# Kernel optimization log

Hardware: AMD Instinct MI355X
Metric: run time of the kernel (lower is better)

## Reference

```python
import jax, jax.numpy as jnp
import numpy as np

HIDDEN = 1024
NUM_HEADS = 16
HEAD_DIM = HIDDEN // NUM_HEADS
EPS = 1e-05


def setup_inputs() -> dict:
    key = jax.random.key(0)
    ks = jax.random.split(key, 6)
    B, S = 4, 2048
    x = jax.random.normal(ks[0], (B, S, HIDDEN), dtype=jnp.float32)
    # trunc_normal_(std=0.02) approximated by scaled normal
    w_in = jax.random.normal(ks[1], (3 * HIDDEN, HIDDEN), dtype=jnp.float32) * 0.02
    b_in = jax.random.normal(ks[2], (3 * HIDDEN,), dtype=jnp.float32) * 0.02
    w_norm = jnp.ones((HIDDEN,), dtype=jnp.float32)
    lim = 1.0 / np.sqrt(HIDDEN)
    w_out = jax.random.uniform(ks[3], (HIDDEN, HIDDEN), dtype=jnp.float32, minval=-lim, maxval=lim)
    b_out = jax.random.uniform(ks[4], (HIDDEN,), dtype=jnp.float32, minval=-lim, maxval=lim)
    return {"x": x, "w_in": w_in, "b_in": b_in, "w_norm": w_norm, "w_out": w_out, "b_out": b_out}


def _rms_norm(x, w, eps):
    var = jnp.mean(jnp.square(x), axis=-1, keepdims=True)
    return x * jax.lax.rsqrt(var + eps) * w


def reference(x, w_in, b_in, w_norm, w_out, b_out):
    B, S, _ = x.shape
    xn = _rms_norm(x, w_norm, EPS)
    qkv = jnp.einsum('bsd,ed->bse', xn, w_in) + b_in  # [B,S,3*HIDDEN]
    q, k, v = jnp.split(qkv, 3, axis=-1)
    # [B,S,H*D] -> [B,H,S,D]
    def split_heads(t):
        return t.reshape(B, S, NUM_HEADS, HEAD_DIM).transpose(0, 2, 1, 3)
    q, k, v = split_heads(q), split_heads(k), split_heads(v)
    scale = 1.0 / np.sqrt(HEAD_DIM)
    scores = jnp.einsum('bhqd,bhkd->bhqk', q, k) * scale
    attn = jax.nn.softmax(scores, axis=-1)
    o = jnp.einsum('bhqk,bhkd->bhqd', attn, v)
    o = o.transpose(0, 2, 1, 3).reshape(B, S, HIDDEN)
    return jnp.einsum('bsd,ed->bse', o, w_out) + b_out
```

## Files before the change

### kernel.cpp

```cpp
#include <hip/hip_runtime.h>
#include <stdint.h>

typedef short bf16x4 __attribute__((ext_vector_type(4)));
typedef short bf16x8 __attribute__((ext_vector_type(8)));
typedef _Float16 f16x8 __attribute__((ext_vector_type(8)));
typedef float f32x4 __attribute__((ext_vector_type(4)));
typedef float f32x16 __attribute__((ext_vector_type(16)));
typedef unsigned int u32x4 __attribute__((ext_vector_type(4)));

#if __has_builtin(__builtin_amdgcn_exp2f)
#define EXP2 __builtin_amdgcn_exp2f
#else
#define EXP2 exp2f
#endif

__device__ __forceinline__ short f2bf(float f) {
  union { float f; uint32_t u; } v; v.f = f;
  uint32_t r = (v.u + 0x7fffu + ((v.u >> 16) & 1u)) >> 16;
  return (short)(uint16_t)r;
}

__device__ __forceinline__ unsigned cvtpk_bf16(float lo, float hi) {
  unsigned r;
  asm("v_cvt_pk_bf16_f32 %0, %1, %2" : "=v"(r) : "v"(lo), "v"(hi));
  return r;
}

__device__ __forceinline__ f32x16 zero16() {
  f32x16 z;
#pragma unroll
  for (int i = 0; i < 16; ++i) z[i] = 0.f;
  return z;
}

__device__ __forceinline__ void gld_lds16(const void* g, void* l) {
  __builtin_amdgcn_global_load_lds(
      (__attribute__((address_space(1))) const void*)g,
      (__attribute__((address_space(3))) void*)l, 16, 0, 0);
}

__global__ __launch_bounds__(256) void k_rmsnorm(const float* __restrict__ x,
                                                 const float* __restrict__ wn,
                                                 short* __restrict__ xn) {
  const int row = blockIdx.x;
  const int t = threadIdx.x;
  const float4 v = reinterpret_cast<const float4*>(x + (size_t)row * 1024)[t];
  float ss = v.x * v.x + v.y * v.y + v.z * v.z + v.w * v.w;
#pragma unroll
  for (int m = 32; m >= 1; m >>= 1) ss += __shfl_xor(ss, m, 64);
  __shared__ float red[4];
  if ((t & 63) == 0) red[t >> 6] = ss;
  __syncthreads();
  const float tot = red[0] + red[1] + red[2] + red[3];
  const float rr = rsqrtf(tot * (1.0f / 1024.0f) + 1e-5f);
  const float4 g = reinterpret_cast<const float4*>(wn)[t];
  bf16x4 o;
  o[0] = f2bf(v.x * rr * g.x);
  o[1] = f2bf(v.y * rr * g.y);
  o[2] = f2bf(v.z * rr * g.z);
  o[3] = f2bf(v.w * rr * g.w);
  reinterpret_cast<bf16x4*>(xn + (size_t)row * 1024)[t] = o;
}

__global__ __launch_bounds__(256) void k_cast_bf(const float* __restrict__ in,
                                                 short* __restrict__ out, int n4) {
  int i = blockIdx.x * 256 + threadIdx.x;
  if (i >= n4) return;
  float4 v = reinterpret_cast<const float4*>(in)[i];
  bf16x4 o;
  o[0] = f2bf(v.x); o[1] = f2bf(v.y); o[2] = f2bf(v.z); o[3] = f2bf(v.w);
  reinterpret_cast<bf16x4*>(out)[i] = o;
}

__global__ __launch_bounds__(256) void k_cast_f16(const float* __restrict__ in,
                                                  _Float16* __restrict__ out, int n4) {
  int i = blockIdx.x * 256 + threadIdx.x;
  if (i >= n4) return;
  float4 v = reinterpret_cast<const float4*>(in)[i];
  _Float16 o[4] = {(_Float16)v.x, (_Float16)v.y, (_Float16)v.z, (_Float16)v.w};
  reinterpret_cast<ulong1*>(out)[i] = *reinterpret_cast<ulong1*>(o);
}

__global__ __launch_bounds__(256) void k_gemm_qkv(const short* __restrict__ A,
                                                  const short* __restrict__ B,
                                                  const float* __restrict__ bias,
                                                  short* __restrict__ qb,
                                                  short* __restrict__ kb,
                                                  short* __restrict__ vb) {
  __shared__ __align__(16) short As[128 * 32];
  __shared__ __align__(16) short Bs[128 * 32];
  const int t = threadIdx.x;
  const long bm0 = (long)blockIdx.y * 128;
  const long bn0 = (long)blockIdx.x * 128;
  const int w = t >> 6, l = t & 63;
  const int wr = (w >> 1) * 64, wc = (w & 1) * 64;
  const int lm = l & 15, h = l >> 4;
  f32x4 acc[4][4];
#pragma unroll
  for (int i = 0; i < 4; ++i)
#pragma unroll
    for (int j = 0; j < 4; ++j) acc[i][j] = (f32x4){0.f, 0.f, 0.f, 0.f};
  const int srow = t >> 2, scol = (t & 3) * 8;
  const short* Ag = A + (bm0 + srow) * 1024 + scol;
  const short* Bg = B + (bn0 + srow) * 1024 + scol;
  short* AsP = As + t * 8;
  short* BsP = Bs + t * 8;
  for (int kt = 0; kt < 32; ++kt) {
    const int k0 = kt << 5;
    gld_lds16(Ag + k0, AsP);
    gld_lds16(Ag + k0 + 64 * 1024, AsP + 2048);
    gld_lds16(Bg + k0, BsP);
    gld_lds16(Bg + k0 + 64 * 1024, BsP + 2048);
    __syncthreads();
    bf16x8 af[4], bfr[4];
#pragma unroll
    for (int mi = 0; mi < 4; ++mi)
      af[mi] = *reinterpret_cast<const bf16x8*>(As + (wr + mi * 16 + lm) * 32 + h * 8);
#pragma unroll
    for (int ni = 0; ni < 4; ++ni)
      bfr[ni] = *reinterpret_cast<const bf16x8*>(Bs + (wc + ni * 16 + lm) * 32 + h * 8);
#pragma unroll
    for (int mi = 0; mi < 4; ++mi)
#pragma unroll
      for (int ni = 0; ni < 4; ++ni)
        acc[mi][ni] = __builtin_amdgcn_mfma_f32_16x16x32_bf16(af[mi], bfr[ni], acc[mi][ni], 0, 0, 0);
    __syncthreads();
  }
#pragma unroll
  for (int ni = 0; ni < 4; ++ni) {
    const int ncol = (int)bn0 + wc + ni * 16 + lm;
    const float bv = bias[ncol];
    const int which = ncol >> 10;
    const int e = ncol & 1023;
#pragma unroll
    for (int mi = 0; mi < 4; ++mi) {
#pragma unroll
      for (int r = 0; r < 4; ++r) {
        const long mrow = bm0 + wr + mi * 16 + h * 4 + r;
        const float val = acc[mi][ni][r] + bv;
        const long off = (((mrow >> 11) * 16 + (e >> 6)) * 2048 + (mrow & 2047)) * 64 + (e & 63);
        if (which == 0) qb[off] = f2bf(val * 0.18033688011112042f);
        else if (which == 1) kb[off] = f2bf(val);
        else vb[off] = f2bf(val);
      }
    }
  }
}

__global__ __launch_bounds__(256) void k_gemm_out(const _Float16* __restrict__ A,
                                                  const _Float16* __restrict__ B,
                                                  const float* __restrict__ bias,
                                                  float* __restrict__ outp) {
  __shared__ __align__(16) _Float16 As[128 * 32];
  __shared__ __align__(16) _Float16 Bs[128 * 32];
  const int t = threadIdx.x;
  const long bm0 = (long)blockIdx.y * 128;
  const long bn0 = (long)blockIdx.x * 128;
  const int w = t >> 6, l = t & 63;
  const int wr = (w >> 1) * 64, wc = (w & 1) * 64;
  const int lm = l & 15, h = l >> 4;
  f32x4 acc[4][4];
#pragma unroll
  for (int i = 0; i < 4; ++i)
#pragma unroll
    for (int j = 0; j < 4; ++j) acc[i][j] = (f32x4){0.f, 0.f, 0.f, 0.f};
  const int srow = t >> 2, scol = (t & 3) * 8;
  const _Float16* Ag = A + (bm0 + srow) * 1024 + scol;
  const _Float16* Bg = B + (bn0 + srow) * 1024 + scol;
  _Float16* AsP = As + t * 8;
  _Float16* BsP = Bs + t * 8;
  for (int kt = 0; kt < 32; ++kt) {
    const int k0 = kt << 5;
    gld_lds16(Ag + k0, AsP);
    gld_lds16(Ag + k0 + 64 * 1024, AsP + 2048);
    gld_lds16(Bg + k0, BsP);
    gld_lds16(Bg + k0 + 64 * 1024, BsP + 2048);
    __syncthreads();
    f16x8 af[4], bfr[4];
#pragma unroll
    for (int mi = 0; mi < 4; ++mi)
      af[mi] = *reinterpret_cast<const f16x8*>(As + (wr + mi * 16 + lm) * 32 + h * 8);
#pragma unroll
    for (int ni = 0; ni < 4; ++ni)
      bfr[ni] = *reinterpret_cast<const f16x8*>(Bs + (wc + ni * 16 + lm) * 32 + h * 8);
#pragma unroll
    for (int mi = 0; mi < 4; ++mi)
#pragma unroll
      for (int ni = 0; ni < 4; ++ni)
        acc[mi][ni] = __builtin_amdgcn_mfma_f32_16x16x32_f16(af[mi], bfr[ni], acc[mi][ni], 0, 0, 0);
    __syncthreads();
  }
#pragma unroll
  for (int ni = 0; ni < 4; ++ni) {
    const int ncol = (int)bn0 + wc + ni * 16 + lm;
    const float bv = bias[ncol];
#pragma unroll
    for (int mi = 0; mi < 4; ++mi) {
#pragma unroll
      for (int r = 0; r < 4; ++r) {
        const long mrow = bm0 + wr + mi * 16 + h * 4 + r;
        outp[mrow * 1024 + ncol] = acc[mi][ni][r] + bv;
      }
    }
  }
}

__global__ __launch_bounds__(256) void k_transpose_v(const short* __restrict__ v,
                                                     short* __restrict__ vt) {
  __shared__ short tile[64][72];
  const int bh = blockIdx.y, st = blockIdx.x;
  const int t = threadIdx.x;
  const int r = t >> 2, c0 = (t & 3) * 16;
  const short* src = v + ((size_t)(bh * 2048 + st * 64 + r)) * 64 + c0;
  bf16x8 a = *reinterpret_cast<const bf16x8*>(src);
  bf16x8 b = *reinterpret_cast<const bf16x8*>(src + 8);
#pragma unroll
  for (int j = 0; j < 8; ++j) tile[r][c0 + j] = a[j];
#pragma unroll
  for (int j = 0; j < 8; ++j) tile[r][c0 + 8 + j] = b[j];
  __syncthreads();
  __align__(16) short tmp[16];
#pragma unroll
  for (int j = 0; j < 16; ++j) tmp[j] = tile[c0 + j][r];
  short* dst = vt + ((size_t)(bh * 64 + r)) * 2048 + st * 64 + c0;
  *reinterpret_cast<bf16x8*>(dst) = *reinterpret_cast<const bf16x8*>(tmp);
  *reinterpret_cast<bf16x8*>(dst + 8) = *reinterpret_cast<const bf16x8*>(tmp + 8);
}

__global__ __launch_bounds__(256) void k_attn(const short* __restrict__ q,
                                              const short* __restrict__ k,
                                              const short* __restrict__ vt,
                                              _Float16* __restrict__ o) {
  __shared__ __align__(16) short Ks[2][4096];
  __shared__ __align__(16) short Vs[2][4096];
  const int bh = blockIdx.y;
  const int qt = blockIdx.x;
  const int t = threadIdx.x;
  const int w = t >> 6, l = t & 63;
  const int lq = l & 31, hh = l >> 5;
  const int xr = lq & 7;
  const int qrow = qt * 128 + w * 32 + lq;

  const short* qp = q + ((size_t)(bh * 2048 + qrow)) * 64 + hh * 8;
  bf16x8 qf[4];
#pragma unroll
  for (int db = 0; db < 4; ++db) qf[db] = *reinterpret_cast<const bf16x8*>(qp + db * 16);

  const int gg0 = w * 128 + l, gg1 = gg0 + 64;
  const int u0 = gg0 ^ ((gg0 >> 3) & 7);
  const int u1 = gg1 ^ ((gg1 >> 3) & 7);
  const short* kh = k + (size_t)bh * 2048 * 64;
  const short* vh = vt + (size_t)bh * 64 * 2048;
  const short* ksrc0 = kh + u0 * 8;
  const short* ksrc1 = kh + u1 * 8;
  const short* vsrc0 = vh + (gg0 >> 3) * 2048 + (u0 & 7) * 8;
  const short* vsrc1 = vh + (gg1 >> 3) * 2048 + (u1 & 7) * 8;

  int koff[2][4], voff[2][4];
#pragma unroll
  for (int ks = 0; ks < 2; ++ks)
#pragma unroll
    for (int db = 0; db < 4; ++db)
      koff[ks][db] = ((ks * 32 + lq) * 8 + ((db * 2 + hh) ^ xr)) * 8;
#pragma unroll
  for (int dt = 0; dt < 2; ++dt)
#pragma unroll
    for (int kg = 0; kg < 4; ++kg)
      voff[dt][kg] = ((dt * 32 + lq) * 8 + ((kg * 2 + hh) ^ xr)) * 8;

  f32x16 oa0 = zero16(), oa1 = zero16();
  float mr = -1e30f, lr = 0.f;

  gld_lds16(ksrc0, &Ks[0][gg0 * 8]);
  gld_lds16(ksrc1, &Ks[0][gg1 * 8]);
  gld_lds16(vsrc0, &Vs[0][gg0 * 8]);
  gld_lds16(vsrc1, &Vs[0][gg1 * 8]);
  __syncthreads();

  int cur = 0;
  for (int kt = 0; kt < 32; ++kt) {
    const int kn = (kt + 1) & 31;
    const int nb = cur ^ 1;
    gld_lds16(ksrc0 + kn * 4096, &Ks[nb][gg0 * 8]);
    gld_lds16(ksrc1 + kn * 4096, &Ks[nb][gg1 * 8]);
    gld_lds16(vsrc0 + kn * 64, &Vs[nb][gg0 * 8]);
    gld_lds16(vsrc1 + kn * 64, &Vs[nb][gg1 * 8]);

    const short* kb_ = Ks[cur];
    const short* vb_ = Vs[cur];
    f32x16 s0 = zero16(), s1 = zero16();
#pragma unroll
    for (int db = 0; db < 4; ++db) {
      bf16x8 kf = *reinterpret_cast<const bf16x8*>(kb_ + koff[0][db]);
      s0 = __builtin_amdgcn_mfma_f32_32x32x16_bf16(kf, qf[db], s0, 0, 0, 0);
    }
#pragma unroll
    for (int db = 0; db < 4; ++db) {
      bf16x8 kf = *reinterpret_cast<const bf16x8*>(kb_ + koff[1][db]);
      s1 = __builtin_amdgcn_mfma_f32_32x32x16_bf16(kf, qf[db], s1, 0, 0, 0);
    }
    float m8[8];
#pragma unroll
    for (int i = 0; i < 8; ++i)
      m8[i] = fmaxf(fmaxf(s0[i], s0[i + 8]), fmaxf(s1[i], s1[i + 8]));
    float m4a = fmaxf(m8[0], m8[4]), m4b = fmaxf(m8[1], m8[5]);
    float m4c = fmaxf(m8[2], m8[6]), m4d = fmaxf(m8[3], m8[7]);
    float tm = fmaxf(fmaxf(m4a, m4b), fmaxf(m4c, m4d));
    tm = fmaxf(tm, __shfl_xor(tm, 32, 64));
    if (!__all(tm <= mr + 8.f)) {
      const float mn = fmaxf(mr, tm);
      const float corr = EXP2(mr - mn);
      lr *= corr;
#pragma unroll
      for (int r = 0; r < 16; ++r) { oa0[r] *= corr; oa1[r] *= corr; }
      mr = mn;
    }
#pragma unroll
    for (int r = 0; r < 16; ++r) {
      s0[r] = EXP2(s0[r] - mr);
      s1[r] = EXP2(s1[r] - mr);
    }
    float a8[8];
#pragma unroll
    for (int i = 0; i < 8; ++i)
      a8[i] = (s0[i] + s0[i + 8]) + (s1[i] + s1[i + 8]);
    float ts = ((a8[0] + a8[4]) + (a8[1] + a8[5])) + ((a8[2] + a8[6]) + (a8[3] + a8[7]));
    ts += __shfl_xor(ts, 32, 64);
    lr += ts;
#pragma unroll
    for (int kg = 0; kg < 4; ++kg) {
      const f32x16& sv = (kg & 2) ? s1 : s0;
      const int b0 = (kg & 1) * 8;
      unsigned w0 = cvtpk_bf16(sv[b0 + 0], sv[b0 + 1]);
      unsigned w2 = cvtpk_bf16(sv[b0 + 4], sv[b0 + 5]);
      unsigned w1 = cvtpk_bf16(sv[b0 + 2], sv[b0 + 3]);
      unsigned w3 = cvtpk_bf16(sv[b0 + 6], sv[b0 + 7]);
      asm("v_permlane32_swap_b32 %0, %1" : "+v"(w0), "+v"(w2));
      asm("v_permlane32_swap_b32 %0, %1" : "+v"(w1), "+v"(w3));
      u32x4 pw = {w0, w1, w2, w3};
      bf16x8 pf = *reinterpret_cast<bf16x8*>(&pw);
      bf16x8 vf0 = *reinterpret_cast<const bf16x8*>(vb_ + voff[0][kg]);
      oa0 = __builtin_amdgcn_mfma_f32_32x32x16_bf16(vf0, pf, oa0, 0, 0, 0);
      bf16x8 vf1 = *reinterpret_cast<const bf16x8*>(vb_ + voff[1][kg]);
      oa1 = __builtin_amdgcn_mfma_f32_32x32x16_bf16(vf1, pf, oa1, 0, 0, 0);
    }
    __syncthreads();
    cur = nb;
  }
  const float inv = 1.0f / lr;
  const int b = bh >> 4, hd = bh & 15;
  _Float16* ob = o + ((size_t)(b * 2048 + qrow)) * 1024 + hd * 64;
#pragma unroll
  for (int r2 = 0; r2 < 16; ++r2) {
    const int d0 = (r2 & 3) + 8 * (r2 >> 2) + 4 * hh;
    ob[d0] = (_Float16)(oa0[r2] * inv);
    ob[d0 + 32] = (_Float16)(oa1[r2] * inv);
  }
}

extern "C" void kernel_launch(void* const* d_in, const int* in_sizes, int n_in,
                              void* d_out, int out_size, void* d_ws, size_t ws_size,
                              hipStream_t stream) {
  const float* x = (const float*)d_in[0];
  const float* w_in = (const float*)d_in[1];
  const float* b_in = (const float*)d_in[2];
  const float* w_norm = (const float*)d_in[3];
  const float* w_out = (const float*)d_in[4];
  const float* b_out = (const float*)d_in[5];
  float* out = (float*)d_out;
  char* ws = (char*)d_ws;
  short* xn = (short*)(ws);
  short* win_b = (short*)(ws + 16777216);
  _Float16* wout_h = (_Float16*)(ws + 23068672);
  short* qb = (short*)(ws + 25165824);
  short* kb = (short*)(ws + 41943040);
  short* vb = (short*)(ws + 58720256);
  short* vt = (short*)(ws + 75497472);
  _Float16* ob = (_Float16*)vb;

  k_cast_bf<<<3072, 256, 0, stream>>>(w_in, win_b, 786432);
  k_cast_f16<<<1024, 256, 0, stream>>>(w_out, wout_h, 262144);
  k_rmsnorm<<<8192, 256, 0, stream>>>(x, w_norm, xn);
  k_gemm_qkv<<<dim3(24, 64), 256, 0, stream>>>(xn, win_b, b_in, qb, kb, vb);
  k_transpose_v<<<dim3(32, 64), 256, 0, stream>>>(vb, vt);
  k_attn<<<dim3(16, 64), 256, 0, stream>>>(qb, kb, vt, ob);
  k_gemm_out<<<dim3(8, 64), 256, 0, stream>>>(ob, wout_h, b_out, out);
}
```

Baseline: 241.6 us.

## Swizzle GEMM block order, add MFMA priority hints, and cheapen softmax reductions

Remaps GEMM block indices so consecutive workgroups share B tiles, which should improve L2 reuse. Wraps MFMA sections in s_setprio so compute-bound waves are scheduled ahead of the others. In attention, the row max uses fmax3 and a permlane32_swap cross-half exchange instead of a shuffle, and the row-sum cross-half reduction is deferred to the end of the loop instead of running every iteration. The permlane swap now goes through a builtin with an inline-asm fallback.

```diff
diff --git a/kernel.cpp b/kernel.cpp
--- a/kernel.cpp
+++ b/kernel.cpp
@@ -7,6 +7,7 @@
 typedef float f32x4 __attribute__((ext_vector_type(4)));
 typedef float f32x16 __attribute__((ext_vector_type(16)));
 typedef unsigned int u32x4 __attribute__((ext_vector_type(4)));
+typedef unsigned int u32x2 __attribute__((ext_vector_type(2)));
 
 #if __has_builtin(__builtin_amdgcn_exp2f)
 #define EXP2 __builtin_amdgcn_exp2f
@@ -24,6 +25,33 @@
   unsigned r;
   asm("v_cvt_pk_bf16_f32 %0, %1, %2" : "=v"(r) : "v"(lo), "v"(hi));
   return r;
+}
+
+#if __has_builtin(__builtin_amdgcn_permlane32_swap)
+__device__ __forceinline__ void plane32_swap(unsigned& a, unsigned& b) {
+  u32x2 r = __builtin_amdgcn_permlane32_swap(a, b, false, false);
+  a = r[0]; b = r[1];
+}
+__device__ __forceinline__ float xhalf_max(float x) {
+  unsigned xu = __builtin_bit_cast(unsigned, x);
+  u32x2 r = __builtin_amdgcn_permlane32_swap(xu, xu, false, false);
+  return fmaxf(__builtin_bit_cast(float, r[0]), __builtin_bit_cast(float, r[1]));
+}
+__device__ __forceinline__ float xhalf_sum(float x) {
+  unsigned xu = __builtin_bit_cast(unsigned, x);
+  u32x2 r = __builtin_amdgcn_permlane32_swap(xu, xu, false, false);
+  return __builtin_bit_cast(float, r[0]) + __builtin_bit_cast(float, r[1]);
+}
+#else
+__device__ __forceinline__ void plane32_swap(unsigned& a, unsigned& b) {
+  asm("s_nop 1\n\tv_permlane32_swap_b32 %0, %1" : "+v"(a), "+v"(b));
+}
+__device__ __forceinline__ float xhalf_max(float x) { return fmaxf(x, __shfl_xor(x, 32, 64)); }
+__device__ __forceinline__ float xhalf_sum(float x) { return x + __shfl_xor(x, 32, 64); }
+#endif
+
+__device__ __forceinline__ float fmax3(float a, float b, float c) {
+  return fmaxf(fmaxf(a, b), c);
 }
 
 __device__ __forceinline__ f32x16 zero16() {
@@ -90,8 +118,10 @@
   __shared__ __align__(16) short As[128 * 32];
   __shared__ __align__(16) short Bs[128 * 32];
   const int t = threadIdx.x;
-  const long bm0 = (long)blockIdx.y * 128;
-  const long bn0 = (long)blockIdx.x * 128;
+  const int orig = blockIdx.y * 24 + blockIdx.x;
+  const int swz = (orig & 7) * 192 + (orig >> 3);
+  const long bn0 = (long)(swz % 24) * 128;
+  const long bm0 = (long)(swz / 24) * 128;
   const int w = t >> 6, l = t & 63;
   const int wr = (w >> 1) * 64, wc = (w & 1) * 64;
   const int lm = l & 15, h = l >> 4;
@@ -119,11 +149,13 @@
 #pragma unroll
     for (int ni = 0; ni < 4; ++ni)
       bfr[ni] = *reinterpret_cast<const bf16x8*>(Bs + (wc + ni * 16 + lm) * 32 + h * 8);
+    __builtin_amdgcn_s_setprio(1);
 #pragma unroll
     for (int mi = 0; mi < 4; ++mi)
 #pragma unroll
       for (int ni = 0; ni < 4; ++ni)
         acc[mi][ni] = __builtin_amdgcn_mfma_f32_16x16x32_bf16(af[mi], bfr[ni], acc[mi][ni], 0, 0, 0);
+    __builtin_amdgcn_s_setprio(0);
     __syncthreads();
   }
 #pragma unroll
@@ -154,8 +186,10 @@
   __shared__ __align__(16) _Float16 As[128 * 32];
   __shared__ __align__(16) _Float16 Bs[128 * 32];
   const int t = threadIdx.x;
-  const long bm0 = (long)blockIdx.y * 128;
-  const long bn0 = (long)blockIdx.x * 128;
+  const int orig = blockIdx.y * 8 + blockIdx.x;
+  const int swz = (orig & 7) * 64 + (orig >> 3);
+  const long bn0 = (long)(swz % 8) * 128;
+  const long bm0 = (long)(swz / 8) * 128;
   const int w = t >> 6, l = t & 63;
   const int wr = (w >> 1) * 64, wc = (w & 1) * 64;
   const int lm = l & 15, h = l >> 4;
@@ -183,11 +217,13 @@
 #pragma unroll
     for (int ni = 0; ni < 4; ++ni)
       bfr[ni] = *reinterpret_cast<const f16x8*>(Bs + (wc + ni * 16 + lm) * 32 + h * 8);
+    __builtin_amdgcn_s_setprio(1);
 #pragma unroll
     for (int mi = 0; mi < 4; ++mi)
 #pragma unroll
       for (int ni = 0; ni < 4; ++ni)
         acc[mi][ni] = __builtin_amdgcn_mfma_f32_16x16x32_f16(af[mi], bfr[ni], acc[mi][ni], 0, 0, 0);
+    __builtin_amdgcn_s_setprio(0);
     __syncthreads();
   }
 #pragma unroll
@@ -289,6 +325,7 @@
     const short* kb_ = Ks[cur];
     const short* vb_ = Vs[cur];
     f32x16 s0 = zero16(), s1 = zero16();
+    __builtin_amdgcn_s_setprio(1);
 #pragma unroll
     for (int db = 0; db < 4; ++db) {
       bf16x8 kf = *reinterpret_cast<const bf16x8*>(kb_ + koff[0][db]);
@@ -299,14 +336,15 @@
       bf16x8 kf = *reinterpret_cast<const bf16x8*>(kb_ + koff[1][db]);
       s1 = __builtin_amdgcn_mfma_f32_32x32x16_bf16(kf, qf[db], s1, 0, 0, 0);
     }
+    __builtin_amdgcn_s_setprio(0);
     float m8[8];
 #pragma unroll
     for (int i = 0; i < 8; ++i)
-      m8[i] = fmaxf(fmaxf(s0[i], s0[i + 8]), fmaxf(s1[i], s1[i + 8]));
-    float m4a = fmaxf(m8[0], m8[4]), m4b = fmaxf(m8[1], m8[5]);
-    float m4c = fmaxf(m8[2], m8[6]), m4d = fmaxf(m8[3], m8[7]);
-    float tm = fmaxf(fmaxf(m4a, m4b), fmaxf(m4c, m4d));
-    tm = fmaxf(tm, __shfl_xor(tm, 32, 64));
+      m8[i] = fmax3(fmaxf(s0[i], s0[i + 8]), s1[i], s1[i + 8]);
+    float t0 = fmax3(m8[0], m8[1], m8[2]);
+    float t1 = fmax3(m8[3], m8[4], m8[5]);
+    float tm = fmax3(fmax3(m8[6], m8[7], t0), t1, -1e30f);
+    tm = xhalf_max(tm);
     if (!__all(tm <= mr + 8.f)) {
       const float mn = fmaxf(mr, tm);
       const float corr = EXP2(mr - mn);
@@ -324,19 +362,18 @@
 #pragma unroll
     for (int i = 0; i < 8; ++i)
       a8[i] = (s0[i] + s0[i + 8]) + (s1[i] + s1[i + 8]);
-    float ts = ((a8[0] + a8[4]) + (a8[1] + a8[5])) + ((a8[2] + a8[6]) + (a8[3] + a8[7]));
-    ts += __shfl_xor(ts, 32, 64);
-    lr += ts;
+    lr += ((a8[0] + a8[4]) + (a8[1] + a8[5])) + ((a8[2] + a8[6]) + (a8[3] + a8[7]));
+    __builtin_amdgcn_s_setprio(1);
 #pragma unroll
     for (int kg = 0; kg < 4; ++kg) {
       const f32x16& sv = (kg & 2) ? s1 : s0;
       const int b0 = (kg & 1) * 8;
       unsigned w0 = cvtpk_bf16(sv[b0 + 0], sv[b0 + 1]);
+      unsigned w1 = cvtpk_bf16(sv[b0 + 2], sv[b0 + 3]);
       unsigned w2 = cvtpk_bf16(sv[b0 + 4], sv[b0 + 5]);
-      unsigned w1 = cvtpk_bf16(sv[b0 + 2], sv[b0 + 3]);
       unsigned w3 = cvtpk_bf16(sv[b0 + 6], sv[b0 + 7]);
-      asm("v_permlane32_swap_b32 %0, %1" : "+v"(w0), "+v"(w2));
-      asm("v_permlane32_swap_b32 %0, %1" : "+v"(w1), "+v"(w3));
+      plane32_swap(w0, w2);
+      plane32_swap(w1, w3);
       u32x4 pw = {w0, w1, w2, w3};
       bf16x8 pf = *reinterpret_cast<bf16x8*>(&pw);
       bf16x8 vf0 = *reinterpret_cast<const bf16x8*>(vb_ + voff[0][kg]);
@@ -344,10 +381,12 @@
       bf16x8 vf1 = *reinterpret_cast<const bf16x8*>(vb_ + voff[1][kg]);
       oa1 = __builtin_amdgcn_mfma_f32_32x32x16_bf16(vf1, pf, oa1, 0, 0, 0);
     }
+    __builtin_amdgcn_s_setprio(0);
     __syncthreads();
     cur = nb;
   }
-  const float inv = 1.0f / lr;
+  const float lt = xhalf_sum(lr);
+  const float inv = 1.0f / lt;
   const int b = bh >> 4, hd = bh & 15;
   _Float16* ob = o + ((size_t)(b * 2048 + qrow)) * 1024 + hd * 64;
 #pragma unroll
```

Result: no change. 241.9 us (+0.1%).
